# Optimization experiments

Measured on AMD Instinct MI355X. Metric: run time of the kernel, lower is better.

The kernel has to match this reference:

```python
import jax, jax.numpy as jnp
import numpy as np

N, NFEAT, NHID, NHEADS, NCLASS = 4096, 64, 64, 4, 64
ALPHA = 0.2        # LeakyReLU negative slope
NEG = -9.0e15      # mask value from the torch code (-9e15)


def _xavier(key, shape, gain=1.414):
    fan_in, fan_out = shape[-2] if len(shape) > 1 else shape[-1], shape[-1]
    if len(shape) == 1:
        fan_in, fan_out = shape[0], 1
    bound = gain * np.sqrt(6.0 / (fan_in + fan_out))
    return jax.random.uniform(key, shape, jnp.float32, -bound, bound)


def setup_inputs() -> dict:
    key = jax.random.key(0)
    ks = jax.random.split(key, 6)
    x = jax.random.normal(ks[0], (N, NFEAT), jnp.float32)
    # sparse-ish adjacency mask with self loops (adj > 0 gating in torch code)
    adj = jax.random.bernoulli(ks[1], 0.02, (N, N)) | jnp.eye(N, dtype=bool)
    W_heads = _xavier(ks[2], (NHEADS, NFEAT, NHID))                  # per-head W
    a_heads = _xavier(ks[3], (NHEADS, 2 * NHID))                     # per-head a (flattened [2F',1])
    W_out = _xavier(ks[4], (NHEADS * NHID, NCLASS))
    a_out = _xavier(ks[5], (2 * NCLASS,))
    return {"x": x, "W_heads": W_heads, "a_heads": a_heads,
            "W_out": W_out, "a_out": a_out, "adj": adj}


def gat_layer(x, adj, W, a, concat):
    # h: [N, F']
    h = x @ W
    Fp = h.shape[-1]
    # e_ij = leakyrelu(a[:F'].h_i + a[F':].h_j)  == torch's cat([h_i, h_j]) @ a
    f1 = h @ a[:Fp]                 # [N]
    f2 = h @ a[Fp:]                 # [N]
    e = jax.nn.leaky_relu(f1[:, None] + f2[None, :], ALPHA)   # [N, N]
    att = jax.nn.softmax(jnp.where(adj, e, NEG), axis=1)      # row softmax over neighbors
    hp = att @ h                    # [N, F']
    return jax.nn.elu(hp) if concat else hp


def reference(x, W_heads, a_heads, W_out, a_out, adj):
    # multi-head GAT with concat (dropout omitted: eval mode)
    heads = jax.vmap(lambda W, a: gat_layer(x, adj, W, a, True))(W_heads, a_heads)  # [H, N, F']
    hcat = jnp.transpose(heads, (1, 0, 2)).reshape(x.shape[0], NHEADS * NHID)       # [N, H*F']
    out = gat_layer(hcat, adj, W_out, a_out, False)                                  # [N, nclass]
    return out
```

## Files before the change

kernel.cpp:

```cpp
#include <hip/hip_runtime.h>

#define N 4096
#define CAP 160
#define ALPHA 0.2f

__device__ __forceinline__ float wred_sum(float v) {
#pragma unroll
  for (int o = 32; o > 0; o >>= 1) v += __shfl_xor(v, o, 64);
  return v;
}

__global__ void stage1_k(const void* __restrict__ adjv, const float* __restrict__ x,
                         const float* __restrict__ W, const float* __restrict__ a,
                         int* __restrict__ cnt, int* __restrict__ cols,
                         float* __restrict__ h1, float* __restrict__ f1h,
                         float* __restrict__ f2h) {
  __shared__ float Ws[64 * 64];
  __shared__ float xs[4][64];
  __shared__ int csh;
  int bid = blockIdx.x;
  int tid = threadIdx.x;
  int lane = tid & 63;
  if (bid < N) {
    int i = bid;
    if (tid == 0) csh = 0;
    __syncthreads();
    int* mycols = cols + (size_t)i * CAP;
    const unsigned char* adjB = (const unsigned char*)adjv;
    bool byteLayout = (adjB[(size_t)N + 1] == 1);
    unsigned long long lt = (lane == 0) ? 0ull : (~0ull >> (64 - lane));
    if (!byteLayout) {
      const int4* row = (const int4*)((const int*)adjv + (size_t)i * N);
      int4 v[4];
#pragma unroll
      for (int it = 0; it < 4; ++it) v[it] = row[tid + it * 256];
#pragma unroll
      for (int it = 0; it < 4; ++it) {
        int b = (tid + it * 256) * 4;
        unsigned long long m0 = __ballot(v[it].x != 0);
        unsigned long long m1 = __ballot(v[it].y != 0);
        unsigned long long m2 = __ballot(v[it].z != 0);
        unsigned long long m3 = __ballot(v[it].w != 0);
        int c0 = __popcll(m0), c1 = __popcll(m1), c2 = __popcll(m2);
        int total = c0 + c1 + c2 + __popcll(m3);
        int wb = 0;
        if (lane == 0 && total) wb = atomicAdd(&csh, total);
        wb = __shfl(wb, 0, 64);
        if (v[it].x) { int p = wb + __popcll(m0 & lt); if (p < CAP) mycols[p] = b; }
        if (v[it].y) { int p = wb + c0 + __popcll(m1 & lt); if (p < CAP) mycols[p] = b + 1; }
        if (v[it].z) { int p = wb + c0 + c1 + __popcll(m2 & lt); if (p < CAP) mycols[p] = b + 2; }
        if (v[it].w) { int p = wb + c0 + c1 + c2 + __popcll(m3 & lt); if (p < CAP) mycols[p] = b + 3; }
      }
    } else {
      const unsigned int* row = (const unsigned int*)(adjB + (size_t)i * N);
      unsigned int v[4];
#pragma unroll
      for (int it = 0; it < 4; ++it) v[it] = row[tid + it * 256];
#pragma unroll
      for (int it = 0; it < 4; ++it) {
        int b = (tid + it * 256) * 4;
        unsigned long long m0 = __ballot((v[it] & 0xffu) != 0);
        unsigned long long m1 = __ballot((v[it] & 0xff00u) != 0);
        unsigned long long m2 = __ballot((v[it] & 0xff0000u) != 0);
        unsigned long long m3 = __ballot((v[it] & 0xff000000u) != 0);
        int c0 = __popcll(m0), c1 = __popcll(m1), c2 = __popcll(m2);
        int total = c0 + c1 + c2 + __popcll(m3);
        int wb = 0;
        if (lane == 0 && total) wb = atomicAdd(&csh, total);
        wb = __shfl(wb, 0, 64);
        if (v[it] & 0xffu) { int p = wb + __popcll(m0 & lt); if (p < CAP) mycols[p] = b; }
        if (v[it] & 0xff00u) { int p = wb + c0 + __popcll(m1 & lt); if (p < CAP) mycols[p] = b + 1; }
        if (v[it] & 0xff0000u) { int p = wb + c0 + c1 + __popcll(m2 & lt); if (p < CAP) mycols[p] = b + 2; }
        if (v[it] & 0xff000000u) { int p = wb + c0 + c1 + c2 + __popcll(m3 & lt); if (p < CAP) mycols[p] = b + 3; }
      }
    }
    __syncthreads();
    if (tid == 0) cnt[i] = min(csh, CAP);
  } else {
    int u = bid - N;
    int h = u & 3;
    int r = tid >> 6, f = lane;
    int n = (u >> 2) * 4 + r;
    for (int t = tid; t < 4096; t += 256) Ws[t] = W[h * 4096 + t];
    xs[r][f] = x[(size_t)n * 64 + f];
    __syncthreads();
    float acc = 0.f;
#pragma unroll
    for (int k = 0; k < 64; ++k) acc = fmaf(xs[r][k], Ws[k * 64 + f], acc);
    h1[((size_t)h * N + n) * 64 + f] = acc;
    float s1 = wred_sum(acc * a[h * 128 + f]);
    float s2 = wred_sum(acc * a[h * 128 + 64 + f]);
    if (f == 0) { f1h[n * 4 + h] = s1; f2h[n * 4 + h] = s2; }
  }
}

__global__ void attn1_gemm_k(const int* __restrict__ cnt, const int* __restrict__ cols,
                             const float* __restrict__ h1,
                             const float* __restrict__ f1g,
                             const float* __restrict__ f2g,
                             const float* __restrict__ Wout,
                             const float* __restrict__ aout,
                             float* __restrict__ h2, float* __restrict__ f1o,
                             float* __restrict__ f2o) {
  int i = blockIdx.x;
  int tid = threadIdx.x;
  int w = tid >> 6, lane = tid & 63;
  __shared__ int cS[CAP];
  __shared__ float pS[4][CAP];
  __shared__ float red[4][4];
  __shared__ float sD[4];
  __shared__ float hrow[256];
  __shared__ float part[4][64];
  int c = cnt[i];
  for (int k = tid; k < c; k += 256) cS[k] = cols[(size_t)i * CAP + k];
  __syncthreads();
  float4 t1 = ((const float4*)f1g)[i];
  float f1i[4] = {t1.x, t1.y, t1.z, t1.w};
  float dloc[4] = {0.f, 0.f, 0.f, 0.f};
  for (int k = tid; k < c; k += 256) {
    float4 t2 = ((const float4*)f2g)[cS[k]];
    float f2v[4] = {t2.x, t2.y, t2.z, t2.w};
#pragma unroll
    for (int h = 0; h < 4; ++h) {
      float s = f1i[h] + f2v[h];
      s = s > 0.f ? s : ALPHA * s;
      float p = __expf(s);
      pS[h][k] = p;
      dloc[h] += p;
    }
  }
#pragma unroll
  for (int h = 0; h < 4; ++h) {
    float d = wred_sum(dloc[h]);
    if (lane == 0) red[w][h] = d;
  }
  __syncthreads();
  if (tid < 4) sD[tid] = red[0][tid] + red[1][tid] + red[2][tid] + red[3][tid];
  __syncthreads();
  int g = lane >> 4, ff = lane & 15, h = w;
  const float* hb = h1 + ((size_t)h * N) * 64;
  float4 acc = {0.f, 0.f, 0.f, 0.f};
#pragma unroll 4
  for (int k0 = 0; k0 < c; k0 += 4) {
    int k = k0 + g;
    bool ok = k < c;
    int j = ok ? cS[k] : 0;
    float p = ok ? pS[h][k] : 0.f;
    float4 v = *(const float4*)(hb + (size_t)j * 64 + ff * 4);
    acc.x = fmaf(p, v.x, acc.x);
    acc.y = fmaf(p, v.y, acc.y);
    acc.z = fmaf(p, v.z, acc.z);
    acc.w = fmaf(p, v.w, acc.w);
  }
#pragma unroll
  for (int o = 16; o < 64; o <<= 1) {
    acc.x += __shfl_xor(acc.x, o, 64);
    acc.y += __shfl_xor(acc.y, o, 64);
    acc.z += __shfl_xor(acc.z, o, 64);
    acc.w += __shfl_xor(acc.w, o, 64);
  }
  if (g == 0) {
    float inv = (c > 0) ? 1.f / sD[h] : 0.f;
    float4 v = {acc.x * inv, acc.y * inv, acc.z * inv, acc.w * inv};
    v.x = v.x > 0.f ? v.x : expm1f(v.x);
    v.y = v.y > 0.f ? v.y : expm1f(v.y);
    v.z = v.z > 0.f ? v.z : expm1f(v.z);
    v.w = v.w > 0.f ? v.w : expm1f(v.w);
    *(float4*)(hrow + h * 64 + ff * 4) = v;
  }
  __syncthreads();
  int f = lane;
  float partial = 0.f;
#pragma unroll 8
  for (int kk = 0; kk < 64; ++kk) {
    int k = w * 64 + kk;
    partial = fmaf(hrow[k], Wout[k * 64 + f], partial);
  }
  part[w][f] = partial;
  __syncthreads();
  if (w == 0) {
    float hv = part[0][f] + part[1][f] + part[2][f] + part[3][f];
    h2[(size_t)i * 64 + f] = hv;
    float s1 = wred_sum(hv * aout[f]);
    float s2 = wred_sum(hv * aout[64 + f]);
    if (f == 0) { f1o[i] = s1; f2o[i] = s2; }
  }
}

__global__ void attn2_k(const int* __restrict__ cnt, const int* __restrict__ cols,
                        const float* __restrict__ h2,
                        const float* __restrict__ f1g,
                        const float* __restrict__ f2g,
                        float* __restrict__ outf) {
  int i = blockIdx.x;
  int tid = threadIdx.x;
  int w = tid >> 6, lane = tid & 63;
  __shared__ int cS[CAP];
  __shared__ float pS[CAP];
  __shared__ float red[4];
  __shared__ float sD;
  __shared__ float4 part4[4][16];
  int c = cnt[i];
  for (int k = tid; k < c; k += 256) cS[k] = cols[(size_t)i * CAP + k];
  __syncthreads();
  float f1i = f1g[i];
  float dloc = 0.f;
  for (int k = tid; k < c; k += 256) {
    float s = f1i + f2g[cS[k]];
    s = s > 0.f ? s : ALPHA * s;
    float p = __expf(s);
    pS[k] = p;
    dloc += p;
  }
  float d = wred_sum(dloc);
  if (lane == 0) red[w] = d;
  __syncthreads();
  if (tid == 0) sD = red[0] + red[1] + red[2] + red[3];
  __syncthreads();
  int g = lane >> 4, ff = lane & 15;
  float4 acc = {0.f, 0.f, 0.f, 0.f};
#pragma unroll 2
  for (int k0 = 0; k0 < c; k0 += 16) {
    int k = k0 + w * 4 + g;
    bool ok = k < c;
    int j = ok ? cS[k] : 0;
    float p = ok ? pS[k] : 0.f;
    float4 v = *(const float4*)(h2 + (size_t)j * 64 + ff * 4);
    acc.x = fmaf(p, v.x, acc.x);
    acc.y = fmaf(p, v.y, acc.y);
    acc.z = fmaf(p, v.z, acc.z);
    acc.w = fmaf(p, v.w, acc.w);
  }
#pragma unroll
  for (int o = 16; o < 64; o <<= 1) {
    acc.x += __shfl_xor(acc.x, o, 64);
    acc.y += __shfl_xor(acc.y, o, 64);
    acc.z += __shfl_xor(acc.z, o, 64);
    acc.w += __shfl_xor(acc.w, o, 64);
  }
  if (g == 0) part4[w][ff] = acc;
  __syncthreads();
  if (w == 0 && g == 0) {
    float4 p0 = part4[0][ff], p1 = part4[1][ff], p2 = part4[2][ff], p3 = part4[3][ff];
    float inv = (c > 0) ? 1.f / sD : 0.f;
    float4 v = {(p0.x + p1.x + p2.x + p3.x) * inv, (p0.y + p1.y + p2.y + p3.y) * inv,
                (p0.z + p1.z + p2.z + p3.z) * inv, (p0.w + p1.w + p2.w + p3.w) * inv};
    *(float4*)(outf + (size_t)i * 64 + ff * 4) = v;
  }
}

extern "C" void kernel_launch(void* const* d_in, const int* in_sizes, int n_in,
                              void* d_out, int out_size, void* d_ws, size_t ws_size,
                              hipStream_t stream) {
  const float* x    = (const float*)d_in[0];
  const float* Wh   = (const float*)d_in[1];
  const float* ah   = (const float*)d_in[2];
  const float* Wout = (const float*)d_in[3];
  const float* aout = (const float*)d_in[4];
  const void*  adj  = d_in[5];

  char* ws = (char*)d_ws;
  int* cnt  = (int*)ws;   ws += (size_t)N * sizeof(int);
  int* cols = (int*)ws;   ws += (size_t)N * CAP * sizeof(int);
  float* h1   = (float*)ws; ws += (size_t)N * 256 * sizeof(float);
  float* f1h  = (float*)ws; ws += (size_t)N * 4 * sizeof(float);
  float* f2h  = (float*)ws; ws += (size_t)N * 4 * sizeof(float);
  float* h2   = (float*)ws; ws += (size_t)N * 64 * sizeof(float);
  float* f1o  = (float*)ws; ws += (size_t)N * sizeof(float);
  float* f2o  = (float*)ws; ws += (size_t)N * sizeof(float);
  (void)in_sizes; (void)n_in; (void)out_size; (void)ws_size;

  stage1_k<<<2 * N, 256, 0, stream>>>(adj, x, Wh, ah, cnt, cols, h1, f1h, f2h);
  attn1_gemm_k<<<N, 256, 0, stream>>>(cnt, cols, h1, f1h, f2h, Wout, aout, h2, f1o, f2o);
  attn2_k<<<N, 256, 0, stream>>>(cnt, cols, h2, f1o, f2o, (float*)d_out);
}
```

Before: 152.3 us.

## Map one wavefront per node in attention kernels and batch four rows per block

Both attention kernels now assign one 64-lane wavefront per destination node, with four nodes per 256-thread block, instead of a whole block per node. This removes most __syncthreads and cross-wave shared-memory reductions, since the softmax denominator is reduced within the wave. In the first kernel each Wout load is reused across four rows of the output projection. The stage1 weight copy into shared memory uses float4 loads. In exchange, each wave now walks all four heads serially in the gather loop, so per-wave latency is longer and there are four times fewer blocks.

```diff
diff --git a/kernel.cpp b/kernel.cpp
--- a/kernel.cpp
+++ b/kernel.cpp
@@ -81,7 +81,9 @@
     int h = u & 3;
     int r = tid >> 6, f = lane;
     int n = (u >> 2) * 4 + r;
-    for (int t = tid; t < 4096; t += 256) Ws[t] = W[h * 4096 + t];
+    const float4* W4 = (const float4*)(W + h * 4096);
+    float4* Ws4 = (float4*)Ws;
+    for (int t = tid; t < 1024; t += 256) Ws4[t] = W4[t];
     xs[r][f] = x[(size_t)n * 64 + f];
     __syncthreads();
     float acc = 0.f;
@@ -102,51 +104,126 @@
                              const float* __restrict__ aout,
                              float* __restrict__ h2, float* __restrict__ f1o,
                              float* __restrict__ f2o) {
-  int i = blockIdx.x;
+  int i0 = blockIdx.x * 4;
   int tid = threadIdx.x;
   int w = tid >> 6, lane = tid & 63;
-  __shared__ int cS[CAP];
-  __shared__ float pS[4][CAP];
-  __shared__ float red[4][4];
-  __shared__ float sD[4];
-  __shared__ float hrow[256];
-  __shared__ float part[4][64];
+  __shared__ int cS[4][CAP];
+  __shared__ float pS[4][4][CAP];
+  __shared__ float hrow[4][256];
+  __shared__ float part[4][4][64];
+  int i = i0 + w;
   int c = cnt[i];
-  for (int k = tid; k < c; k += 256) cS[k] = cols[(size_t)i * CAP + k];
-  __syncthreads();
+  for (int k = lane; k < c; k += 64) cS[w][k] = cols[(size_t)i * CAP + k];
   float4 t1 = ((const float4*)f1g)[i];
   float f1i[4] = {t1.x, t1.y, t1.z, t1.w};
   float dloc[4] = {0.f, 0.f, 0.f, 0.f};
-  for (int k = tid; k < c; k += 256) {
-    float4 t2 = ((const float4*)f2g)[cS[k]];
+  for (int k = lane; k < c; k += 64) {
+    float4 t2 = ((const float4*)f2g)[cS[w][k]];
     float f2v[4] = {t2.x, t2.y, t2.z, t2.w};
 #pragma unroll
     for (int h = 0; h < 4; ++h) {
       float s = f1i[h] + f2v[h];
       s = s > 0.f ? s : ALPHA * s;
       float p = __expf(s);
-      pS[h][k] = p;
+      pS[w][h][k] = p;
       dloc[h] += p;
     }
   }
+  float dinv[4];
 #pragma unroll
   for (int h = 0; h < 4; ++h) {
     float d = wred_sum(dloc[h]);
-    if (lane == 0) red[w][h] = d;
+    dinv[h] = (c > 0) ? 1.f / d : 0.f;
+  }
+  int g = lane >> 4, ff = lane & 15;
+#pragma unroll
+  for (int h = 0; h < 4; ++h) {
+    const float* hb = h1 + ((size_t)h * N) * 64;
+    float4 acc = {0.f, 0.f, 0.f, 0.f};
+#pragma unroll 4
+    for (int k0 = 0; k0 < c; k0 += 4) {
+      int k = k0 + g;
+      bool ok = k < c;
+      int j = ok ? cS[w][k] : 0;
+      float p = ok ? pS[w][h][k] : 0.f;
+      float4 v = *(const float4*)(hb + (size_t)j * 64 + ff * 4);
+      acc.x = fmaf(p, v.x, acc.x);
+      acc.y = fmaf(p, v.y, acc.y);
+      acc.z = fmaf(p, v.z, acc.z);
+      acc.w = fmaf(p, v.w, acc.w);
+    }
+#pragma unroll
+    for (int o = 16; o < 64; o <<= 1) {
+      acc.x += __shfl_xor(acc.x, o, 64);
+      acc.y += __shfl_xor(acc.y, o, 64);
+      acc.z += __shfl_xor(acc.z, o, 64);
+      acc.w += __shfl_xor(acc.w, o, 64);
+    }
+    if (g == 0) {
+      float4 v = {acc.x * dinv[h], acc.y * dinv[h], acc.z * dinv[h], acc.w * dinv[h]};
+      v.x = v.x > 0.f ? v.x : expm1f(v.x);
+      v.y = v.y > 0.f ? v.y : expm1f(v.y);
+      v.z = v.z > 0.f ? v.z : expm1f(v.z);
+      v.w = v.w > 0.f ? v.w : expm1f(v.w);
+      *(float4*)(&hrow[w][h * 64 + ff * 4]) = v;
+    }
   }
   __syncthreads();
-  if (tid < 4) sD[tid] = red[0][tid] + red[1][tid] + red[2][tid] + red[3][tid];
+  int f = lane;
+  float p0 = 0.f, p1 = 0.f, p2 = 0.f, p3 = 0.f;
+#pragma unroll 8
+  for (int kk = 0; kk < 64; ++kk) {
+    int k = w * 64 + kk;
+    float wv = Wout[k * 64 + f];
+    p0 = fmaf(hrow[0][k], wv, p0);
+    p1 = fmaf(hrow[1][k], wv, p1);
+    p2 = fmaf(hrow[2][k], wv, p2);
+    p3 = fmaf(hrow[3][k], wv, p3);
+  }
+  part[w][0][f] = p0;
+  part[w][1][f] = p1;
+  part[w][2][f] = p2;
+  part[w][3][f] = p3;
   __syncthreads();
-  int g = lane >> 4, ff = lane & 15, h = w;
-  const float* hb = h1 + ((size_t)h * N) * 64;
+  float hv = part[0][w][lane] + part[1][w][lane] + part[2][w][lane] + part[3][w][lane];
+  h2[(size_t)i * 64 + lane] = hv;
+  float s1 = wred_sum(hv * aout[lane]);
+  float s2 = wred_sum(hv * aout[64 + lane]);
+  if (lane == 0) { f1o[i] = s1; f2o[i] = s2; }
+}
+
+__global__ void attn2_k(const int* __restrict__ cnt, const int* __restrict__ cols,
+                        const float* __restrict__ h2,
+                        const float* __restrict__ f1g,
+                        const float* __restrict__ f2g,
+                        float* __restrict__ outf) {
+  int tid = threadIdx.x;
+  int w = tid >> 6, lane = tid & 63;
+  int i = blockIdx.x * 4 + w;
+  __shared__ int cS[4][CAP];
+  __shared__ float pS[4][CAP];
+  int c = cnt[i];
+  for (int k = lane; k < c; k += 64) cS[w][k] = cols[(size_t)i * CAP + k];
+  float f1i = f1g[i];
+  float dloc = 0.f;
+  for (int k = lane; k < c; k += 64) {
+    float s = f1i + f2g[cS[w][k]];
+    s = s > 0.f ? s : ALPHA * s;
+    float p = __expf(s);
+    pS[w][k] = p;
+    dloc += p;
+  }
+  float d = wred_sum(dloc);
+  float inv = (c > 0) ? 1.f / d : 0.f;
+  int g = lane >> 4, ff = lane & 15;
   float4 acc = {0.f, 0.f, 0.f, 0.f};
 #pragma unroll 4
   for (int k0 = 0; k0 < c; k0 += 4) {
     int k = k0 + g;
     bool ok = k < c;
-    int j = ok ? cS[k] : 0;
-    float p = ok ? pS[h][k] : 0.f;
-    float4 v = *(const float4*)(hb + (size_t)j * 64 + ff * 4);
+    int j = ok ? cS[w][k] : 0;
+    float p = ok ? pS[w][k] : 0.f;
+    float4 v = *(const float4*)(h2 + (size_t)j * 64 + ff * 4);
     acc.x = fmaf(p, v.x, acc.x);
     acc.y = fmaf(p, v.y, acc.y);
     acc.z = fmaf(p, v.z, acc.z);
@@ -160,91 +237,7 @@
     acc.w += __shfl_xor(acc.w, o, 64);
   }
   if (g == 0) {
-    float inv = (c > 0) ? 1.f / sD[h] : 0.f;
     float4 v = {acc.x * inv, acc.y * inv, acc.z * inv, acc.w * inv};
-    v.x = v.x > 0.f ? v.x : expm1f(v.x);
-    v.y = v.y > 0.f ? v.y : expm1f(v.y);
-    v.z = v.z > 0.f ? v.z : expm1f(v.z);
-    v.w = v.w > 0.f ? v.w : expm1f(v.w);
-    *(float4*)(hrow + h * 64 + ff * 4) = v;
-  }
-  __syncthreads();
-  int f = lane;
-  float partial = 0.f;
-#pragma unroll 8
-  for (int kk = 0; kk < 64; ++kk) {
-    int k = w * 64 + kk;
-    partial = fmaf(hrow[k], Wout[k * 64 + f], partial);
-  }
-  part[w][f] = partial;
-  __syncthreads();
-  if (w == 0) {
-    float hv = part[0][f] + part[1][f] + part[2][f] + part[3][f];
-    h2[(size_t)i * 64 + f] = hv;
-    float s1 = wred_sum(hv * aout[f]);
-    float s2 = wred_sum(hv * aout[64 + f]);
-    if (f == 0) { f1o[i] = s1; f2o[i] = s2; }
-  }
-}
-
-__global__ void attn2_k(const int* __restrict__ cnt, const int* __restrict__ cols,
-                        const float* __restrict__ h2,
-                        const float* __restrict__ f1g,
-                        const float* __restrict__ f2g,
-                        float* __restrict__ outf) {
-  int i = blockIdx.x;
-  int tid = threadIdx.x;
-  int w = tid >> 6, lane = tid & 63;
-  __shared__ int cS[CAP];
-  __shared__ float pS[CAP];
-  __shared__ float red[4];
-  __shared__ float sD;
-  __shared__ float4 part4[4][16];
-  int c = cnt[i];
-  for (int k = tid; k < c; k += 256) cS[k] = cols[(size_t)i * CAP + k];
-  __syncthreads();
-  float f1i = f1g[i];
-  float dloc = 0.f;
-  for (int k = tid; k < c; k += 256) {
-    float s = f1i + f2g[cS[k]];
-    s = s > 0.f ? s : ALPHA * s;
-    float p = __expf(s);
-    pS[k] = p;
-    dloc += p;
-  }
-  float d = wred_sum(dloc);
-  if (lane == 0) red[w] = d;
-  __syncthreads();
-  if (tid == 0) sD = red[0] + red[1] + red[2] + red[3];
-  __syncthreads();
-  int g = lane >> 4, ff = lane & 15;
-  float4 acc = {0.f, 0.f, 0.f, 0.f};
-#pragma unroll 2
-  for (int k0 = 0; k0 < c; k0 += 16) {
-    int k = k0 + w * 4 + g;
-    bool ok = k < c;
-    int j = ok ? cS[k] : 0;
-    float p = ok ? pS[k] : 0.f;
-    float4 v = *(const float4*)(h2 + (size_t)j * 64 + ff * 4);
-    acc.x = fmaf(p, v.x, acc.x);
-    acc.y = fmaf(p, v.y, acc.y);
-    acc.z = fmaf(p, v.z, acc.z);
-    acc.w = fmaf(p, v.w, acc.w);
-  }
-#pragma unroll
-  for (int o = 16; o < 64; o <<= 1) {
-    acc.x += __shfl_xor(acc.x, o, 64);
-    acc.y += __shfl_xor(acc.y, o, 64);
-    acc.z += __shfl_xor(acc.z, o, 64);
-    acc.w += __shfl_xor(acc.w, o, 64);
-  }
-  if (g == 0) part4[w][ff] = acc;
-  __syncthreads();
-  if (w == 0 && g == 0) {
-    float4 p0 = part4[0][ff], p1 = part4[1][ff], p2 = part4[2][ff], p3 = part4[3][ff];
-    float inv = (c > 0) ? 1.f / sD : 0.f;
-    float4 v = {(p0.x + p1.x + p2.x + p3.x) * inv, (p0.y + p1.y + p2.y + p3.y) * inv,
-                (p0.z + p1.z + p2.z + p3.z) * inv, (p0.w + p1.w + p2.w + p3.w) * inv};
     *(float4*)(outf + (size_t)i * 64 + ff * 4) = v;
   }
 }
@@ -271,6 +264,7 @@
   (void)in_sizes; (void)n_in; (void)out_size; (void)ws_size;
 
   stage1_k<<<2 * N, 256, 0, stream>>>(adj, x, Wh, ah, cnt, cols, h1, f1h, f2h);
-  attn1_gemm_k<<<N, 256, 0, stream>>>(cnt, cols, h1, f1h, f2h, Wout, aout, h2, f1o, f2o);
-  attn2_k<<<N, 256, 0, stream>>>(cnt, cols, h2, f1o, f2o, (float*)d_out);
-}
+  attn1_gemm_k<<<N / 4, 256, 0, stream>>>(cnt, cols, h1, f1h, f2h, Wout, aout,
+                                          h2, f1o, f2o);
+  attn2_k<<<N / 4, 256, 0, stream>>>(cnt, cols, h2, f1o, f2o, (float*)d_out);
+}
```

After: 162.8 us. +6.9%, slower.
